# Optimization experiments

Measured on AMD Instinct MI355X. Metric: run time of the kernel, lower is better.

The kernel has to match this reference:

```python
import jax, jax.numpy as jnp
import numpy as np

NUM_LAYER = 5
EMB = 300
N_NODES = 100000
N_EDGES = 250000
BN_EPS = 1e-5


def setup_inputs() -> dict:
    key = jax.random.key(0)
    ks = jax.random.split(key, 12)
    s = 0.05
    inp = {
        "x": jax.random.randint(ks[0], (N_NODES, 2), 0, 3),
        "edge_index": jax.random.randint(ks[1], (2, N_EDGES), 0, N_NODES),
        "edge_attr": jax.random.randint(ks[2], (N_EDGES, 2), 0, 3),
        # node-feature embedding tables
        "x_emb1": jax.random.normal(ks[3], (120, EMB), jnp.float32) * s,
        "x_emb2": jax.random.normal(ks[4], (3, EMB), jnp.float32) * s,
        # per-layer edge embedding tables (bond type=6, bond direction=3)
        "e_emb1": jax.random.normal(ks[5], (NUM_LAYER, 6, EMB), jnp.float32) * s,
        "e_emb2": jax.random.normal(ks[6], (NUM_LAYER, 3, EMB), jnp.float32) * s,
        # per-layer GIN MLP: Linear(D,2D) -> ReLU -> Linear(2D,D); weights stored (out,in)
        "w1": jax.random.normal(ks[7], (NUM_LAYER, 2 * EMB, EMB), jnp.float32) * s,
        "b1": jnp.zeros((NUM_LAYER, 2 * EMB), jnp.float32),
        "w2": jax.random.normal(ks[8], (NUM_LAYER, EMB, 2 * EMB), jnp.float32) * s,
        "b2": jnp.zeros((NUM_LAYER, EMB), jnp.float32),
        # per-layer BatchNorm1d affine params (training-mode batch stats)
        "gamma": jnp.ones((NUM_LAYER, EMB), jnp.float32),
        "beta": jnp.zeros((NUM_LAYER, EMB), jnp.float32),
    }
    return inp


def reference(x, edge_index, edge_attr, x_emb1, x_emb2, e_emb1, e_emb2, w1, b1, w2, b2, gamma, beta):
    n = x.shape[0]
    # input node embedding: atom type + chirality tag
    h = x_emb1[x[:, 0]] + x_emb2[x[:, 1]]  # [N, D]

    # add self loops (self-loop edge_attr = [4, 0])
    loop = jnp.arange(n, dtype=edge_index.dtype)
    src = jnp.concatenate([edge_index[0], loop])  # [E+N]
    dst = jnp.concatenate([edge_index[1], loop])
    ea0 = jnp.concatenate([edge_attr[:, 0], jnp.full((n,), 4, edge_attr.dtype)])
    ea1 = jnp.concatenate([edge_attr[:, 1], jnp.zeros((n,), edge_attr.dtype)])

    for l in range(NUM_LAYER):
        e = e_emb1[l][ea0] + e_emb2[l][ea1]           # [E+N, D] edge embeddings
        msg = h[src] + e                               # gather + message
        agg = jax.ops.segment_sum(msg, dst, num_segments=n)  # scatter-add aggregate
        hid = jnp.maximum(agg @ w1[l].T + b1[l], 0.0)  # GIN MLP
        h2 = hid @ w2[l].T + b2[l]
        # BatchNorm1d (training-mode batch statistics, biased variance)
        mu = h2.mean(axis=0)
        var = jnp.mean((h2 - mu) ** 2, axis=0)
        h2 = (h2 - mu) * jax.lax.rsqrt(var + BN_EPS) * gamma[l] + beta[l]
        if l < NUM_LAYER - 1:
            h2 = jnp.maximum(h2, 0.0)  # ReLU (dropout ratio = 0)
        h = h2

    # JK == 'last'
    return h
```

## Files before the change

### kernel.cpp

```cpp
#include <hip/hip_runtime.h>
#include <hip/hip_bf16.h>

#define DD 300
#define C4 75
#define CG 40
#define AGS 320
#define HS 320
#define ECS 320
#define BN_EPS 1e-5f

typedef _Float16 f16x8 __attribute__((ext_vector_type(8)));
typedef float f32x4 __attribute__((ext_vector_type(4)));

union PackH4 { _Float16 h[4]; uint2 u; };

__device__ __forceinline__ void gld_lds16(const void* g, void* lds) {
    __builtin_amdgcn_global_load_lds(
        (const __attribute__((address_space(1))) void*)g,
        (__attribute__((address_space(3))) void*)lds, 16, 0, 0);
}

__global__ __launch_bounds__(256) void embed_kernel(
    const int* __restrict__ x, const float* __restrict__ emb1,
    const float* __restrict__ emb2, _Float16* __restrict__ h, int total4)
{
    int i = blockIdx.x * 256 + threadIdx.x;
    if (i >= total4) return;
    int node = i / C4, chunk = i - node * C4;
    int a = x[2 * node], b = x[2 * node + 1];
    int c = chunk << 2;
    float4 v1 = *(const float4*)(emb1 + (size_t)a * DD + c);
    float4 v2 = *(const float4*)(emb2 + (size_t)b * DD + c);
    PackH4 p;
    p.h[0] = (_Float16)(v1.x + v2.x);
    p.h[1] = (_Float16)(v1.y + v2.y);
    p.h[2] = (_Float16)(v1.z + v2.z);
    p.h[3] = (_Float16)(v1.w + v2.w);
    *(uint2*)(h + (size_t)node * HS + c) = p.u;
}

__global__ __launch_bounds__(256) void build_ec_kernel(
    const float* __restrict__ e1, const float* __restrict__ e2, float* __restrict__ ec)
{
    int gid = blockIdx.x * 256 + threadIdx.x;
    if (gid >= 5 * 18 * ECS) return;
    int l = gid / (18 * ECS);
    int rem = gid - l * 18 * ECS;
    int combo = rem / ECS;
    int c = rem - combo * ECS;
    int a0 = combo / 3, a1 = combo - a0 * 3;
    float v = 0.f;
    if (c < DD)
        v = e1[(size_t)l * 6 * DD + a0 * DD + c] + e2[(size_t)l * 3 * DD + a1 * DD + c];
    ec[gid] = v;
}

__global__ __launch_bounds__(256) void deg_kernel(
    const int* __restrict__ ei, int* __restrict__ deg, int E)
{
    int e = blockIdx.x * 256 + threadIdx.x;
    if (e >= E) return;
    atomicAdd(&deg[ei[E + e]], 1);
}

__global__ __launch_bounds__(256) void scan1_kernel(
    const int* __restrict__ deg, int* __restrict__ pre, int* __restrict__ blockSum, int n)
{
    __shared__ int sa[256], sb[256];
    int t = threadIdx.x;
    int base = blockIdx.x * 1024 + t * 4;
    int v0 = (base + 0 < n) ? deg[base + 0] : 0;
    int v1 = (base + 1 < n) ? deg[base + 1] : 0;
    int v2 = (base + 2 < n) ? deg[base + 2] : 0;
    int v3 = (base + 3 < n) ? deg[base + 3] : 0;
    int tot = v0 + v1 + v2 + v3;
    sa[t] = tot;
    __syncthreads();
    int* src = sa; int* dst = sb;
    for (int off = 1; off < 256; off <<= 1) {
        int v = src[t];
        if (t >= off) v += src[t - off];
        dst[t] = v;
        __syncthreads();
        int* tmp = src; src = dst; dst = tmp;
    }
    int incl = src[t];
    int excl = incl - tot;
    if (base + 0 < n) pre[base + 0] = excl;
    if (base + 1 < n) pre[base + 1] = excl + v0;
    if (base + 2 < n) pre[base + 2] = excl + v0 + v1;
    if (base + 3 < n) pre[base + 3] = excl + v0 + v1 + v2;
    if (t == 255) blockSum[blockIdx.x] = incl;
}

__global__ __launch_bounds__(256) void scan2_kernel(int* __restrict__ blockSum, int nb)
{
    __shared__ int sa[256], sb[256];
    int t = threadIdx.x;
    int v = (t < nb) ? blockSum[t] : 0;
    sa[t] = v;
    __syncthreads();
    int* src = sa; int* dst = sb;
    for (int off = 1; off < 256; off <<= 1) {
        int x = src[t];
        if (t >= off) x += src[t - off];
        dst[t] = x;
        __syncthreads();
        int* tmp = src; src = dst; dst = tmp;
    }
    if (t < nb) blockSum[t] = src[t] - v;
}

__global__ __launch_bounds__(256) void scan3_kernel(
    const int* __restrict__ pre, const int* __restrict__ blockSum,
    int* __restrict__ rowPtr, int* __restrict__ cursor, int n, int E)
{
    int idx = blockIdx.x * 256 + threadIdx.x;
    if (idx > n) return;
    int v = (idx < n) ? pre[idx] + blockSum[idx >> 10] : E;
    rowPtr[idx] = v;
    if (idx < n) cursor[idx] = v;
}

__global__ __launch_bounds__(256) void fill_kernel(
    const int* __restrict__ ei, const int* __restrict__ ea,
    int* __restrict__ cursor, int* __restrict__ edges, int E)
{
    int e = blockIdx.x * 256 + threadIdx.x;
    if (e >= E) return;
    int src = ei[e];
    int dst = ei[E + e];
    int combo = ea[2 * e] * 3 + ea[2 * e + 1];
    int slot = atomicAdd(&cursor[dst], 1);
    edges[slot] = src | (combo << 18);
}

__global__ __launch_bounds__(256) void gather_kernel(
    const _Float16* __restrict__ h, const int* __restrict__ rowPtr,
    const int* __restrict__ edges, const float* __restrict__ ec,
    const float* __restrict__ scale, const float* __restrict__ shift, int use_affine,
    _Float16* __restrict__ agg, int n)
{
    int gid = blockIdx.x * 256 + threadIdx.x;
    int node = gid / CG, ch = gid - node * CG;
    if (node >= n) return;
    int c = ch << 3;

    float s[8], t[8];
    if (use_affine) {
        *(float4*)&s[0] = *(const float4*)(scale + c);
        *(float4*)&s[4] = *(const float4*)(scale + c + 4);
        *(float4*)&t[0] = *(const float4*)(shift + c);
        *(float4*)&t[4] = *(const float4*)(shift + c + 4);
    }

    float a[8];
    {
        f16x8 hv = *(const f16x8*)(h + (size_t)node * HS + c);
#pragma unroll
        for (int k = 0; k < 8; ++k) {
            float v = (float)hv[k];
            if (use_affine) v = fmaxf(fmaf(s[k], v, t[k]), 0.f);
            a[k] = v;
        }
        float e0[8];
        *(float4*)&e0[0] = *(const float4*)(ec + 12 * ECS + c);
        *(float4*)&e0[4] = *(const float4*)(ec + 12 * ECS + c + 4);
#pragma unroll
        for (int k = 0; k < 8; ++k) a[k] += e0[k];
    }

    int e = rowPtr[node];
    const int end = rowPtr[node + 1];
    for (; e < end; ++e) {
        int pk = edges[e];
        int src = pk & 0x3FFFF;
        int combo = pk >> 18;
        f16x8 hv = *(const f16x8*)(h + (size_t)src * HS + c);
        float ev[8];
        *(float4*)&ev[0] = *(const float4*)(ec + combo * ECS + c);
        *(float4*)&ev[4] = *(const float4*)(ec + combo * ECS + c + 4);
#pragma unroll
        for (int k = 0; k < 8; ++k) {
            float v = (float)hv[k];
            if (use_affine) v = fmaxf(fmaf(s[k], v, t[k]), 0.f);
            a[k] += v + ev[k];
        }
    }

    f16x8 o;
#pragma unroll
    for (int k = 0; k < 8; ++k) o[k] = (_Float16)a[k];
    *(f16x8*)(agg + (size_t)node * AGS + c) = o;
}

__global__ __launch_bounds__(256) void convert_w_kernel(
    const float* __restrict__ w, _Float16* __restrict__ wf,
    int rows, int cols, int rowsP, int colsP)
{
    int gid = blockIdx.x * 256 + threadIdx.x;
    int total = 5 * rowsP * colsP;
    if (gid >= total) return;
    int l = gid / (rowsP * colsP);
    int rem = gid - l * (rowsP * colsP);
    int r = rem / colsP;
    int k = rem - r * colsP;
    float v = (r < rows && k < cols) ? w[((size_t)l * rows + r) * cols + k] : 0.f;
    wf[gid] = (_Float16)v;
}

template <bool RELU, bool DO_STATS>
__global__ __launch_bounds__(256, 4) void mfma_gemm_lds(
    const _Float16* __restrict__ A, const _Float16* __restrict__ W,
    const float* __restrict__ bias, _Float16* __restrict__ out,
    float* __restrict__ sum, float* __restrict__ sumsq,
    int M, int Kp, int outStride, int outN, int nCol)
{
    __shared__ __attribute__((aligned(16))) unsigned short sA[64 * 64];
    __shared__ __attribute__((aligned(16))) unsigned short sB[128 * 64];

    const int bid = blockIdx.x;
    const int group = bid / (8 * nCol);
    const int within = bid - group * 8 * nCol;
    const int rowT = group * 8 + (within & 7);
    const int colT = within >> 3;
    const int bm = rowT << 6;
    const int bn = colT << 7;

    const int tid = threadIdx.x;
    const int lane = tid & 63, wv = tid >> 6;
    const int wy = wv & 1, wx = wv >> 1;
    const int quad = lane >> 4, l16 = lane & 15;

    const int r8 = lane >> 3;
    const int chv = (lane & 7) ^ r8;

    f32x4 acc[2][4] = {};

    for (int k0 = 0; k0 < Kp; k0 += 64) {
        __syncthreads();
#pragma unroll
        for (int j = 0; j < 2; ++j) {
            int rloc = wv * 16 + j * 8 + r8;
            gld_lds16(A + (size_t)(bm + rloc) * Kp + k0 + chv * 8,
                      &sA[(wv * 16 + j * 8) * 64]);
        }
#pragma unroll
        for (int j = 0; j < 4; ++j) {
            int rloc = wv * 32 + j * 8 + r8;
            gld_lds16(W + (size_t)(bn + rloc) * Kp + k0 + chv * 8,
                      &sB[(wv * 32 + j * 8) * 64]);
        }
        __syncthreads();
#pragma unroll
        for (int kk = 0; kk < 2; ++kk) {
            f16x8 a[2], b[4];
#pragma unroll
            for (int i = 0; i < 2; ++i) {
                int rA = wy * 32 + i * 16 + l16;
                int slotA = (kk * 4 + quad) ^ (rA & 7);
                a[i] = *(const f16x8*)&sA[rA * 64 + slotA * 8];
            }
#pragma unroll
            for (int j = 0; j < 4; ++j) {
                int rB = wx * 64 + j * 16 + l16;
                int slotB = (kk * 4 + quad) ^ (rB & 7);
                b[j] = *(const f16x8*)&sB[rB * 64 + slotB * 8];
            }
#pragma unroll
            for (int i = 0; i < 2; ++i)
#pragma unroll
                for (int j = 0; j < 4; ++j)
                    acc[i][j] = __builtin_amdgcn_mfma_f32_16x16x32_f16(
                        a[i], b[j], acc[i][j], 0, 0, 0);
        }
    }

#pragma unroll
    for (int j = 0; j < 4; ++j) {
        int col = bn + wx * 64 + j * 16 + l16;
        float bv = (col < outN) ? bias[col] : 0.f;
        float cs = 0.f, cq = 0.f;
#pragma unroll
        for (int i = 0; i < 2; ++i) {
            int rowBase = bm + wy * 32 + i * 16 + (quad << 2);
#pragma unroll
            for (int r = 0; r < 4; ++r) {
                int row = rowBase + r;
                if (row >= M) continue;
                float v = acc[i][j][r] + bv;
                if constexpr (DO_STATS) { if (col < outN) { cs += v; cq += v * v; } }
                float o;
                if constexpr (RELU) o = (col < outN) ? fmaxf(v, 0.f) : 0.f;
                else                o = (col < outN) ? v : 0.f;
                if (col < outStride)
                    out[(size_t)row * outStride + col] = (_Float16)o;
            }
        }
        if constexpr (DO_STATS) {
            cs += __shfl_down(cs, 32); cq += __shfl_down(cq, 32);
            cs += __shfl_down(cs, 16); cq += __shfl_down(cq, 16);
            if (quad == 0 && col < outN) {
                atomicAdd(&sum[col], cs);
                atomicAdd(&sumsq[col], cq);
            }
        }
    }
}

__global__ void finalize_kernel(
    const float* __restrict__ sum, const float* __restrict__ sumsq,
    const float* __restrict__ gamma, const float* __restrict__ beta,
    float* __restrict__ scale, float* __restrict__ shift, float inv_n)
{
    int c = threadIdx.x;
    if (c < DD) {
        float mu = sum[c] * inv_n;
        float var = sumsq[c] * inv_n - mu * mu;
        float inv = rsqrtf(var + BN_EPS);
        float sc = gamma[c] * inv;
        scale[c] = sc;
        shift[c] = fmaf(-mu, sc, beta[c]);
    } else if (c < 320) {
        scale[c] = 0.f;
        shift[c] = 0.f;
    }
}

__global__ __launch_bounds__(256) void apply_kernel(
    const _Float16* __restrict__ h, const float* __restrict__ scale,
    const float* __restrict__ shift, float* __restrict__ out, int total4)
{
    int i = blockIdx.x * 256 + threadIdx.x;
    if (i >= total4) return;
    int node = i / C4;
    int c = (i - node * C4) << 2;
    PackH4 ph; ph.u = *(const uint2*)(h + (size_t)node * HS + c);
    float4 r;
    r.x = fmaf(scale[c + 0], (float)ph.h[0], shift[c + 0]);
    r.y = fmaf(scale[c + 1], (float)ph.h[1], shift[c + 1]);
    r.z = fmaf(scale[c + 2], (float)ph.h[2], shift[c + 2]);
    r.w = fmaf(scale[c + 3], (float)ph.h[3], shift[c + 3]);
    ((float4*)out)[i] = r;
}

extern "C" void kernel_launch(void* const* d_in, const int* in_sizes, int n_in,
                              void* d_out, int out_size, void* d_ws, size_t ws_size,
                              hipStream_t stream)
{
    const int*   x      = (const int*)d_in[0];
    const int*   ei     = (const int*)d_in[1];
    const int*   ea     = (const int*)d_in[2];
    const float* x_emb1 = (const float*)d_in[3];
    const float* x_emb2 = (const float*)d_in[4];
    const float* e_emb1 = (const float*)d_in[5];
    const float* e_emb2 = (const float*)d_in[6];
    const float* w1     = (const float*)d_in[7];
    const float* b1     = (const float*)d_in[8];
    const float* w2     = (const float*)d_in[9];
    const float* b2     = (const float*)d_in[10];
    const float* gamma  = (const float*)d_in[11];
    const float* beta   = (const float*)d_in[12];

    const int n = in_sizes[0] / 2;
    const int E = in_sizes[1] / 2;
    const int nRowT = (n + 63) / 64;
    const int nRowTP = ((nRowT + 7) / 8) * 8;
    const int MpA = nRowTP * 64;
    const int Kp1 = AGS, Kp2 = 640;
    const int NP1 = 640, NP2 = 384;

    char* p = (char*)d_ws;
    auto alloc = [&](size_t bytes) -> void* {
        void* r = (void*)p;
        p += (bytes + 255) & ~(size_t)255;
        return r;
    };
    _Float16* agg  = (_Float16*)alloc((size_t)MpA * Kp1 * 2);
    _Float16* hid  = (_Float16*)alloc((size_t)MpA * Kp2 * 2);
    _Float16* h    = (_Float16*)alloc((size_t)n * HS * 2);
    _Float16* w1f  = (_Float16*)alloc((size_t)5 * NP1 * Kp1 * 2);
    _Float16* w2f  = (_Float16*)alloc((size_t)5 * NP2 * Kp2 * 2);
    float* ec     = (float*)alloc((size_t)5 * 18 * ECS * 4);
    int*   deg    = (int*)alloc((size_t)n * 4);
    int*   rowPtr = (int*)alloc((size_t)(n + 1) * 4);
    int*   cursor = (int*)alloc((size_t)n * 4);
    int*   blockSum = (int*)alloc(256 * 4);
    int*   edges  = (int*)alloc((size_t)E * 4);
    float* sum   = (float*)alloc(320 * 4);
    float* sumsq = (float*)alloc(320 * 4);
    float* scale = (float*)alloc(320 * 4);
    float* shift = (float*)alloc(320 * 4);

    const int total4 = n * C4;
    const int nb = (n + 1023) / 1024;

    {
        convert_w_kernel<<<(5 * NP1 * Kp1 + 255) / 256, 256, 0, stream>>>(w1, w1f, 600, 300, NP1, Kp1);
        convert_w_kernel<<<(5 * NP2 * Kp2 + 255) / 256, 256, 0, stream>>>(w2, w2f, 300, 600, NP2, Kp2);
        build_ec_kernel<<<(5 * 18 * ECS + 255) / 256, 256, 0, stream>>>(e_emb1, e_emb2, ec);
        hipMemsetAsync(deg, 0, (size_t)n * 4, stream);
        deg_kernel<<<(E + 255) / 256, 256, 0, stream>>>(ei, deg, E);
        scan1_kernel<<<nb, 256, 0, stream>>>(deg, cursor , blockSum, n);
        scan2_kernel<<<1, 256, 0, stream>>>(blockSum, nb);
        scan3_kernel<<<(n + 256) / 256, 256, 0, stream>>>(cursor, blockSum, rowPtr, deg , n, E);
        fill_kernel<<<(E + 255) / 256, 256, 0, stream>>>(ei, ea, deg, edges, E);
        hipMemsetAsync(agg, 0, (size_t)MpA * Kp1 * 2, stream);
        hipMemsetAsync(h, 0, (size_t)n * HS * 2, stream);
        embed_kernel<<<(total4 + 255) / 256, 256, 0, stream>>>(x, x_emb1, x_emb2, h, total4);
    }

    const int gatherTotal = n * CG;
    const int nCol1 = NP1 / 128;
    const int nCol2 = NP2 / 128;
    const int g1 = nRowTP * nCol1;
    const int g2 = nRowTP * nCol2;

    for (int l = 0; l < 5; l++) {
        hipMemsetAsync(sum, 0, 2 * 320 * sizeof(float), stream);
        gather_kernel<<<(gatherTotal + 255) / 256, 256, 0, stream>>>(
            h, rowPtr, edges, ec + (size_t)l * 18 * ECS, scale, shift, l > 0 ? 1 : 0,
            agg, n);
        mfma_gemm_lds<true, false><<<g1, 256, 0, stream>>>(
            agg, w1f + (size_t)l * NP1 * Kp1,
            b1 + (size_t)l * 600, hid, nullptr, nullptr,
            n, Kp1, Kp2, 600, nCol1);
        mfma_gemm_lds<false, true><<<g2, 256, 0, stream>>>(
            hid, w2f + (size_t)l * NP2 * Kp2,
            b2 + (size_t)l * 300, h, sum, sumsq,
            n, Kp2, HS, 300, nCol2);
        finalize_kernel<<<1, 320, 0, stream>>>(sum, sumsq, gamma + (size_t)l * DD,
                                               beta + (size_t)l * DD, scale, shift,
                                               1.0f / (float)n);
    }
    apply_kernel<<<(total4 + 255) / 256, 256, 0, stream>>>(h, scale, shift,
                                                           (float*)d_out, total4);
}
```

Baseline: 1.558 ms.

## Multi-buffer GEMM LDS tiles with async prefetch and explicit vmcnt waits

Reworks the MFMA GEMM main loop so the A tile is triple-buffered and the B tile double-buffered in LDS. Loads for the next K steps are issued ahead with global_load_lds, and manual s_waitcnt vmcnt counts plus raw barriers replace the previous sync-load-sync pattern. The aim is to hide global memory latency behind MFMA work. In exchange LDS use rises to about 56KB per block, so launch bounds drop to 2 blocks per CU, and correctness now depends on hand-counted vmcnt values.

```diff
diff --git a/kernel.cpp b/kernel.cpp
--- a/kernel.cpp
+++ b/kernel.cpp
@@ -210,14 +210,14 @@
 }
 
 template <bool RELU, bool DO_STATS>
-__global__ __launch_bounds__(256, 4) void mfma_gemm_lds(
+__global__ __launch_bounds__(256, 2) void mfma_gemm_lds(
     const _Float16* __restrict__ A, const _Float16* __restrict__ W,
     const float* __restrict__ bias, _Float16* __restrict__ out,
     float* __restrict__ sum, float* __restrict__ sumsq,
     int M, int Kp, int outStride, int outN, int nCol)
 {
-    __shared__ __attribute__((aligned(16))) unsigned short sA[64 * 64];
-    __shared__ __attribute__((aligned(16))) unsigned short sB[128 * 64];
+    __shared__ __attribute__((aligned(16))) unsigned short sA[3][64 * 64];
+    __shared__ __attribute__((aligned(16))) unsigned short sB[2][128 * 64];
 
     const int bid = blockIdx.x;
     const int group = bid / (8 * nCol);
@@ -237,21 +237,45 @@
 
     f32x4 acc[2][4] = {};
 
-    for (int k0 = 0; k0 < Kp; k0 += 64) {
-        __syncthreads();
+    auto STAGE_A = [&](int buf, int k0) {
 #pragma unroll
         for (int j = 0; j < 2; ++j) {
             int rloc = wv * 16 + j * 8 + r8;
             gld_lds16(A + (size_t)(bm + rloc) * Kp + k0 + chv * 8,
-                      &sA[(wv * 16 + j * 8) * 64]);
-        }
+                      &sA[buf][(wv * 16 + j * 8) * 64]);
+        }
+    };
+    auto STAGE_B = [&](int buf, int k0) {
 #pragma unroll
         for (int j = 0; j < 4; ++j) {
             int rloc = wv * 32 + j * 8 + r8;
             gld_lds16(W + (size_t)(bn + rloc) * Kp + k0 + chv * 8,
-                      &sB[(wv * 32 + j * 8) * 64]);
-        }
-        __syncthreads();
+                      &sB[buf][(wv * 32 + j * 8) * 64]);
+        }
+    };
+
+    const int nT = Kp >> 6;
+    STAGE_A(0, 0);
+    STAGE_A(1, 64);
+    STAGE_B(0, 0);
+
+    for (int t = 0; t < nT; ++t) {
+        if (t + 1 < nT) STAGE_B((t + 1) & 1, (t + 1) << 6);
+        if (t + 2 < nT) STAGE_A((t + 2) % 3, (t + 2) << 6);
+        if (t == 0) {
+            asm volatile("s_waitcnt vmcnt(6)" ::: "memory");
+        } else if (t + 2 < nT) {
+            asm volatile("s_waitcnt vmcnt(8)" ::: "memory");
+        } else if (t + 1 < nT) {
+            asm volatile("s_waitcnt vmcnt(6)" ::: "memory");
+        } else {
+            asm volatile("s_waitcnt vmcnt(0)" ::: "memory");
+        }
+        __builtin_amdgcn_s_barrier();
+        __builtin_amdgcn_sched_barrier(0);
+
+        const unsigned short* sAp = &sA[t % 3][0];
+        const unsigned short* sBp = &sB[t & 1][0];
 #pragma unroll
         for (int kk = 0; kk < 2; ++kk) {
             f16x8 a[2], b[4];
@@ -259,13 +283,13 @@
             for (int i = 0; i < 2; ++i) {
                 int rA = wy * 32 + i * 16 + l16;
                 int slotA = (kk * 4 + quad) ^ (rA & 7);
-                a[i] = *(const f16x8*)&sA[rA * 64 + slotA * 8];
+                a[i] = *(const f16x8*)&sAp[rA * 64 + slotA * 8];
             }
 #pragma unroll
             for (int j = 0; j < 4; ++j) {
                 int rB = wx * 64 + j * 16 + l16;
                 int slotB = (kk * 4 + quad) ^ (rB & 7);
-                b[j] = *(const f16x8*)&sB[rB * 64 + slotB * 8];
+                b[j] = *(const f16x8*)&sBp[rB * 64 + slotB * 8];
             }
 #pragma unroll
             for (int i = 0; i < 2; ++i)
@@ -274,6 +298,8 @@
                     acc[i][j] = __builtin_amdgcn_mfma_f32_16x16x32_f16(
                         a[i], b[j], acc[i][j], 0, 0, 0);
         }
+        __builtin_amdgcn_s_barrier();
+        __builtin_amdgcn_sched_barrier(0);
     }
 
 #pragma unroll
```

Result: slower. 1.900 ms (+22.0%).
